# Kernel tuning notes

Measured on AMD Instinct MI355X. Metric: run time of the kernel, lower is better.

## Reference

```python
import jax, jax.numpy as jnp
import numpy as np
import math

VOCAB, D, L, B, S = 32000, 1024, 6, 4, 1024
FF = 4 * D


def sinusoidal_pe(max_len, d_model):
    pos = np.arange(max_len)[:, None].astype(np.float32)
    div = np.exp(np.arange(0, d_model, 2).astype(np.float32) * (-math.log(10000.0) / d_model))
    pe = np.zeros((max_len, d_model), dtype=np.float32)
    pe[:, 0::2] = np.sin(pos * div)
    pe[:, 1::2] = np.cos(pos * div)
    return jnp.asarray(pe)


def layernorm(x, g, b, eps=1e-5):
    mu = jnp.mean(x, axis=-1, keepdims=True)
    var = jnp.mean(jnp.square(x - mu), axis=-1, keepdims=True)
    return (x - mu) * jax.lax.rsqrt(var + eps) * g + b


def setup_inputs() -> dict:
    key = jax.random.key(0)
    ks = jax.random.split(key, 16)
    s = 0.02
    inp = {
        "input_ids": jax.random.randint(ks[0], (B, S), 0, VOCAB, dtype=jnp.int32),
        "attention_mask": jnp.ones((B, S), dtype=jnp.int32),
        "emb": jax.random.normal(ks[1], (VOCAB, D), jnp.float32) * s,
        "Wq": jax.random.normal(ks[2], (L, D, D), jnp.float32) * s,
        "Wk": jax.random.normal(ks[3], (L, D, D), jnp.float32) * s,
        "Wv": jax.random.normal(ks[4], (L, D, D), jnp.float32) * s,
        "bq": jnp.zeros((L, D), jnp.float32),
        "bk": jnp.zeros((L, D), jnp.float32),
        "bv": jnp.zeros((L, D), jnp.float32),
        "g1": jnp.ones((L, D), jnp.float32),
        "beta1": jnp.zeros((L, D), jnp.float32),
        "Wf1": jax.random.normal(ks[5], (L, D, FF), jnp.float32) * s,
        "bf1": jnp.zeros((L, FF), jnp.float32),
        "Wf2": jax.random.normal(ks[6], (L, FF, D), jnp.float32) * s,
        "bf2": jnp.zeros((L, D), jnp.float32),
        "g2": jnp.ones((L, D), jnp.float32),
        "beta2": jnp.zeros((L, D), jnp.float32),
    }
    return inp


def reference(input_ids, attention_mask, emb, Wq, Wk, Wv, bq, bk, bv,
              g1, beta1, Wf1, bf1, Wf2, bf2, g2, beta2):
    pe = sinusoidal_pe(1024, D)
    x = emb[input_ids] + pe[: input_ids.shape[1]]           # [B,S,D]
    mask = (attention_mask[:, None, :] != 0)                # [B,1,S]
    scale = 1.0 / math.sqrt(D)
    for l in range(L):
        Q = jnp.einsum('bsd,de->bse', x, Wq[l]) + bq[l]
        K = jnp.einsum('bsd,de->bse', x, Wk[l]) + bk[l]
        V = jnp.einsum('bsd,de->bse', x, Wv[l]) + bv[l]
        scores = jnp.einsum('bqd,bkd->bqk', Q, K) * scale   # [B,S,S]
        scores = jnp.where(mask, scores, -1e9)
        attn = jax.nn.softmax(scores, axis=-1)
        a = jnp.einsum('bqk,bkd->bqd', attn, V)
        x = layernorm(x + a, g1[l], beta1[l])
        h = jax.nn.relu(jnp.einsum('bsd,df->bsf', x, Wf1[l]) + bf1[l])
        f = jnp.einsum('bsf,fd->bsd', h, Wf2[l]) + bf2[l]
        x = layernorm(x + f, g2[l], beta2[l])
    return x
```

## Files before the change

### kernel.cpp

```cpp
#include <hip/hip_runtime.h>

typedef __bf16 bf16_t;
typedef __bf16 bf16x8 __attribute__((ext_vector_type(8)));
typedef float f32x4 __attribute__((ext_vector_type(4)));
typedef unsigned short u16;

#define DEV static __device__ __forceinline__

DEV float bf2f(u16 u) { __bf16 h = __builtin_bit_cast(__bf16, u); return (float)h; }
DEV u16 f2bf(float f) { __bf16 h = (__bf16)f; return __builtin_bit_cast(u16, h); }

DEV void gll16(bf16_t* lds, const bf16_t* g) {
    __builtin_amdgcn_global_load_lds(
        (const __attribute__((address_space(1))) void*)g,
        (__attribute__((address_space(3))) void*)lds, 16, 0, 0);
}

#define WAITV(N) asm volatile("s_waitcnt vmcnt(" #N ")" ::: "memory")

template <int EPI>
__global__ __launch_bounds__(512, 1)
void gemm8p(const bf16_t* __restrict__ A, int lda,
            const bf16_t* __restrict__ Bt, int ldb,
            bf16_t* __restrict__ C, int ldc,
            const float* __restrict__ bias, int K,
            long kadv, long cadv)
{
    __shared__ bf16_t Asm[2 * 2 * 8192];
    __shared__ bf16_t Bsm[2 * 2 * 8192];
    const int tid = threadIdx.x, w = tid >> 6, l = tid & 63;
    const int z = blockIdx.z;
    A  += (size_t)z * kadv;
    Bt += (size_t)z * kadv;
    C  += (size_t)z * cadv;

    const int gx = gridDim.x;
    int lin = blockIdx.y * gx + blockIdx.x;
    const int nlin = gx * gridDim.y;
    lin = (lin & 7) * (nlin >> 3) + (lin >> 3);
    const size_t row0 = (size_t)(lin / gx) * 256;
    const size_t col0 = (size_t)(lin % gx) * 256;

    const int wr = w >> 2, wc = w & 3;
    const int bh = wc >> 1;
    const int browoff = (wc & 1) * 64;
    const int fr = l & 15, q = l >> 4, sw = l & 7;

    const int srow = w * 8 + (l >> 3);
    const int sslot8 = ((l & 7) ^ ((l >> 3) & 7)) * 8;
    const bf16_t* AgH0 = A  + (row0 + srow) * (size_t)lda + sslot8;
    const bf16_t* BgH0 = Bt + (col0 + srow) * (size_t)ldb + sslot8;
    const size_t a128 = (size_t)128 * lda, b128 = (size_t)128 * ldb;
    const size_t a64  = (size_t)64 * lda,  b64  = (size_t)64 * ldb;
    const int wlds = w * 512;

#define STAGE_PAIR(buf, tt, p)                                                 \
    do {                                                                       \
        const int koff = (tt) * 64;                                            \
        if ((p) == 0) {                                                        \
            gll16(Asm + ((buf)*2+0)*8192 + wlds,        AgH0 + koff);          \
            gll16(Asm + ((buf)*2+0)*8192 + 4096 + wlds, AgH0 + koff + a64);    \
        } else if ((p) == 1) {                                                 \
            gll16(Asm + ((buf)*2+1)*8192 + wlds,        AgH0 + a128 + koff);   \
            gll16(Asm + ((buf)*2+1)*8192 + 4096 + wlds, AgH0 + a128 + koff + a64); \
        } else if ((p) == 2) {                                                 \
            gll16(Bsm + ((buf)*2+0)*8192 + wlds,        BgH0 + koff);          \
            gll16(Bsm + ((buf)*2+0)*8192 + 4096 + wlds, BgH0 + koff + b64);    \
        } else {                                                               \
            gll16(Bsm + ((buf)*2+1)*8192 + wlds,        BgH0 + b128 + koff);   \
            gll16(Bsm + ((buf)*2+1)*8192 + 4096 + wlds, BgH0 + b128 + koff + b64); \
        }                                                                      \
    } while (0)

    f32x4 acc[8][4] = {};
    const int NT = K >> 6;

    STAGE_PAIR(0, 0, 0); STAGE_PAIR(0, 0, 1); STAGE_PAIR(0, 0, 2); STAGE_PAIR(0, 0, 3);
    if (NT > 1) { STAGE_PAIR(1, 1, 0); WAITV(2); } else { WAITV(0); }
    __builtin_amdgcn_sched_barrier(0);
    __builtin_amdgcn_s_barrier();

    for (int t = 0; t < NT; ++t) {
        const int cur = t & 1, nxt = cur ^ 1;
        const bool hasN1 = (t + 1 < NT), hasN2 = (t + 2 < NT);
        const bf16_t* Ab = Asm + (cur * 2 + wr) * 8192;
        const bf16_t* Bb = Bsm + (cur * 2 + bh) * 8192;

        bf16x8 aR[4][2], bR[4][2];
#pragma unroll
        for (int mi = 0; mi < 4; mi++)
#pragma unroll
            for (int kk = 0; kk < 2; kk++)
                aR[mi][kk] = *(const bf16x8*)&Ab[(mi * 16 + fr) * 64 + ((kk * 4 + q) ^ sw) * 8];
#pragma unroll
        for (int ni = 0; ni < 4; ni++)
#pragma unroll
            for (int kk = 0; kk < 2; kk++)
                bR[ni][kk] = *(const bf16x8*)&Bb[(browoff + ni * 16 + fr) * 64 + ((kk * 4 + q) ^ sw) * 8];
        if (hasN1) { STAGE_PAIR(nxt, t + 1, 1); STAGE_PAIR(nxt, t + 1, 2); }
        __builtin_amdgcn_s_setprio(1);
#pragma unroll
        for (int mi = 0; mi < 4; mi++)
#pragma unroll
            for (int ni = 0; ni < 4; ni++)
#pragma unroll
                for (int kk = 0; kk < 2; kk++)
                    acc[mi][ni] = __builtin_amdgcn_mfma_f32_16x16x32_bf16(aR[mi][kk], bR[ni][kk], acc[mi][ni], 0, 0, 0);
        __builtin_amdgcn_s_setprio(0);

        bf16x8 a2[4][2];
#pragma unroll
        for (int mi = 0; mi < 4; mi++)
#pragma unroll
            for (int kk = 0; kk < 2; kk++)
                a2[mi][kk] = *(const bf16x8*)&Ab[((4 + mi) * 16 + fr) * 64 + ((kk * 4 + q) ^ sw) * 8];
        if (hasN1) STAGE_PAIR(nxt, t + 1, 3);
        __builtin_amdgcn_s_setprio(1);
#pragma unroll
        for (int mi = 0; mi < 4; mi++)
#pragma unroll
            for (int ni = 0; ni < 4; ni++)
#pragma unroll
                for (int kk = 0; kk < 2; kk++)
                    acc[4 + mi][ni] = __builtin_amdgcn_mfma_f32_16x16x32_bf16(a2[mi][kk], bR[ni][kk], acc[4 + mi][ni], 0, 0, 0);
        __builtin_amdgcn_s_setprio(0);

        __builtin_amdgcn_s_barrier();
        if (hasN2) STAGE_PAIR(cur, t + 2, 0);
        if (hasN1) {
            if (hasN2) { WAITV(2); } else { WAITV(0); }
            __builtin_amdgcn_sched_barrier(0);
        }
        __builtin_amdgcn_s_barrier();
    }
#undef STAGE_PAIR

    const int cr = q * 4, cc = fr;
#pragma unroll
    for (int ni = 0; ni < 4; ni++) {
        size_t c = col0 + wc * 64 + ni * 16 + cc;
        float bv = bias ? bias[c] : 0.f;
#pragma unroll
        for (int mi = 0; mi < 8; mi++) {
            size_t r = row0 + wr * 128 + mi * 16 + cr;
#pragma unroll
            for (int j = 0; j < 4; j++) {
                float v = acc[mi][ni][j] + bv;
                if (EPI == 1) v = fmaxf(v, 0.f);
                C[(r + j) * ldc + c] = (bf16_t)v;
            }
        }
    }
}

template <int EPI>
__global__ __launch_bounds__(256)
void gemm_db(const bf16_t* __restrict__ A, int lda, long sA,
             const bf16_t* __restrict__ Bt, int ldb, long sB,
             void* __restrict__ Cv, int ldc, long sC,
             const float* __restrict__ bias, int K, float scale)
{
    __shared__ bf16_t Asm[2][128 * 64];
    __shared__ bf16_t Bsm[2][128 * 64];
    const int tid = threadIdx.x, w = tid >> 6, l = tid & 63;
    const int bz = blockIdx.z;

    const int gx = gridDim.x;
    int lin = blockIdx.y * gx + blockIdx.x;
    const int nlin = gx * gridDim.y;
    lin = (lin & 7) * (nlin >> 3) + (lin >> 3);
    const size_t row0 = (size_t)(lin / gx) * 128;
    const size_t col0 = (size_t)(lin % gx) * 128;

    A  += (size_t)bz * sA;
    Bt += (size_t)bz * sB;

    const int lr = l >> 3;
    const int sl = (l & 7) ^ lr;
    const bf16_t* Ag = A  + (row0 + (size_t)(w * 32) + lr) * lda + sl * 8;
    const bf16_t* Bg = Bt + (col0 + (size_t)(w * 32) + lr) * ldb + sl * 8;
    const int wlds = (w * 32) * 64;

#define STA(buf, tt)                                                           \
    do { const int ko = (tt) * 64;                                             \
        _Pragma("unroll")                                                      \
        for (int c = 0; c < 4; c++)                                            \
            gll16(&Asm[buf][wlds + c * 8 * 64], Ag + (size_t)(c * 8) * lda + ko); \
    } while (0)
#define STB(buf, tt)                                                           \
    do { const int ko = (tt) * 64;                                             \
        _Pragma("unroll")                                                      \
        for (int c = 0; c < 4; c++)                                            \
            gll16(&Bsm[buf][wlds + c * 8 * 64], Bg + (size_t)(c * 8) * ldb + ko); \
    } while (0)

    const int wm = (w >> 1) * 64, wn = (w & 1) * 64;
    const int fr16 = l & 15, q4 = l >> 4, sw = l & 7;
    f32x4 acc[4][4] = {};
    const int NT = K >> 6;

    STA(0, 0); STB(0, 0);
    if (NT > 1) { STA(1, 1); WAITV(4); } else { WAITV(0); }
    __builtin_amdgcn_sched_barrier(0);
    __builtin_amdgcn_s_barrier();

    for (int t = 0; t < NT; ++t) {
        const int cur = t & 1, nxt = cur ^ 1;
        const bool hasN1 = (t + 1 < NT), hasN2 = (t + 2 < NT);

        bf16x8 a0[4], b0[4], a1[4], b1[4];
        const int s0 = (q4 ^ sw) * 8, s1 = ((4 + q4) ^ sw) * 8;
#pragma unroll
        for (int i = 0; i < 4; i++) {
            a0[i] = *(const bf16x8*)&Asm[cur][(wm + i * 16 + fr16) * 64 + s0];
            b0[i] = *(const bf16x8*)&Bsm[cur][(wn + i * 16 + fr16) * 64 + s0];
        }
        if (hasN1) STB(nxt, t + 1);
        __builtin_amdgcn_s_setprio(1);
#pragma unroll
        for (int mi = 0; mi < 4; mi++)
#pragma unroll
            for (int ni = 0; ni < 4; ni++)
                acc[mi][ni] = __builtin_amdgcn_mfma_f32_16x16x32_bf16(a0[mi], b0[ni], acc[mi][ni], 0, 0, 0);
        __builtin_amdgcn_s_setprio(0);
#pragma unroll
        for (int i = 0; i < 4; i++) {
            a1[i] = *(const bf16x8*)&Asm[cur][(wm + i * 16 + fr16) * 64 + s1];
            b1[i] = *(const bf16x8*)&Bsm[cur][(wn + i * 16 + fr16) * 64 + s1];
        }
        __builtin_amdgcn_s_setprio(1);
#pragma unroll
        for (int mi = 0; mi < 4; mi++)
#pragma unroll
            for (int ni = 0; ni < 4; ni++)
                acc[mi][ni] = __builtin_amdgcn_mfma_f32_16x16x32_bf16(a1[mi], b1[ni], acc[mi][ni], 0, 0, 0);
        __builtin_amdgcn_s_setprio(0);

        __builtin_amdgcn_s_barrier();
        if (hasN2) STA(cur, t + 2);
        if (hasN1) {
            if (hasN2) { WAITV(4); } else { WAITV(0); }
            __builtin_amdgcn_sched_barrier(0);
        }
        __builtin_amdgcn_s_barrier();
    }
#undef STA
#undef STB

    const int cr = q4 * 4, cc = fr16;
    if (EPI == 2) {
        float* C = (float*)Cv + (size_t)bz * sC;
#pragma unroll
        for (int mi = 0; mi < 4; mi++)
#pragma unroll
            for (int ni = 0; ni < 4; ni++) {
                size_t r = row0 + wm + mi * 16 + cr;
                size_t c = col0 + wn + ni * 16 + cc;
#pragma unroll
                for (int j = 0; j < 4; j++)
                    C[(r + j) * ldc + c] = acc[mi][ni][j] * scale;
            }
    } else {
        bf16_t* C = (bf16_t*)Cv + (size_t)bz * sC;
#pragma unroll
        for (int ni = 0; ni < 4; ni++) {
            size_t c = col0 + wn + ni * 16 + cc;
            float bv = bias ? bias[c] : 0.f;
#pragma unroll
            for (int mi = 0; mi < 4; mi++) {
                size_t r = row0 + wm + mi * 16 + cr;
#pragma unroll
                for (int j = 0; j < 4; j++) {
                    float v = acc[mi][ni][j] + bv;
                    if (EPI == 1) v = fmaxf(v, 0.f);
                    C[(r + j) * ldc + c] = (bf16_t)v;
                }
            }
        }
    }
}

__global__ __launch_bounds__(256)
void prep_kernel(const float* __restrict__ Wq, const float* __restrict__ Wk,
                 const float* __restrict__ Wv, const float* __restrict__ Wf1,
                 const float* __restrict__ Wf2,
                 const float* __restrict__ bq, const float* __restrict__ bk,
                 const float* __restrict__ bv,
                 const int* __restrict__ ids, const float* __restrict__ emb,
                 bf16_t* __restrict__ wqkvTA, bf16_t* __restrict__ wf1TA,
                 bf16_t* __restrict__ wf2TA, float* __restrict__ qbiasA,
                 float* __restrict__ x, bf16_t* __restrict__ xb)
{
    __shared__ bf16_t tls[64][72];
    const size_t DD = 1024 * 1024;
    int id = blockIdx.x;
    if (id < 16896) {
        const float* src; bf16_t* dst; int ldin, ldout, bx, by;
        if (id < 4608) {
            int layer = id / 768, r = id % 768, which = r >> 8, t = r & 255;
            src = (which == 0 ? Wq : which == 1 ? Wk : Wv) + (size_t)layer * DD;
            dst = wqkvTA + (size_t)layer * 3 * DD + (size_t)which * DD;
            ldin = 1024; ldout = 1024; bx = (t & 15) * 64; by = (t >> 4) * 64;
        } else if (id < 10752) {
            int i = id - 4608, layer = i >> 10, t = i & 1023;
            src = Wf1 + (size_t)layer * 4 * DD; dst = wf1TA + (size_t)layer * 4 * DD;
            ldin = 4096; ldout = 1024; bx = (t & 63) * 64; by = (t >> 6) * 64;
        } else {
            int i = id - 10752, layer = i >> 10, t = i & 1023;
            src = Wf2 + (size_t)layer * 4 * DD; dst = wf2TA + (size_t)layer * 4 * DD;
            ldin = 1024; ldout = 4096; bx = (t & 15) * 64; by = (t >> 4) * 64;
        }
        const int tid = threadIdx.x;
        const int cj = (tid & 15) * 4, ri = tid >> 4;
#pragma unroll
        for (int k = 0; k < 4; k++) {
            int r = ri + k * 16;
            float4 v = *(const float4*)&src[(size_t)(by + r) * ldin + bx + cj];
            ushort4 o = {f2bf(v.x), f2bf(v.y), f2bf(v.z), f2bf(v.w)};
            *(ushort4*)&tls[r][cj] = o;
        }
        __syncthreads();
#pragma unroll
        for (int k = 0; k < 4; k++) {
            int i2 = ri + k * 16;
            ushort4 o;
            o.x = __builtin_bit_cast(u16, tls[cj + 0][i2]);
            o.y = __builtin_bit_cast(u16, tls[cj + 1][i2]);
            o.z = __builtin_bit_cast(u16, tls[cj + 2][i2]);
            o.w = __builtin_bit_cast(u16, tls[cj + 3][i2]);
            *(ushort4*)&dst[(size_t)(bx + i2) * ldout + by + cj] = o;
        }
        return;
    }
    id -= 16896;
    if (id < 72) {
        int i = id * 256 + threadIdx.x;
        int lyr = i / 3072, j = i - lyr * 3072;
        qbiasA[i] = (j < 1024) ? bq[lyr * 1024 + j]
                  : (j < 2048) ? bk[lyr * 1024 + j - 1024]
                               : bv[lyr * 1024 + j - 2048];
        return;
    }
    id -= 72;
    const int row = id;
    const int s = row & 1023;
    const int eid = ids[row];
    const float* er = emb + (size_t)eid * 1024;
    float* xr = x + (size_t)row * 1024;
    bf16_t* br = xb + (size_t)row * 1024;
#pragma unroll
    for (int k = 0; k < 2; k++) {
        int i = threadIdx.x + 256 * k;
        int d = 2 * i;
        float dv = expf((float)d * -0.008994473019508f);
        float ph = (float)s * dv;
        float sv, cv;
        sincosf(ph, &sv, &cv);
        float2 ev = *(const float2*)&er[d];
        float x0 = ev.x + sv;
        float x1 = ev.y + cv;
        float2 xo = {x0, x1};
        *(float2*)&xr[d] = xo;
        ushort2 bo = {f2bf(x0), f2bf(x1)};
        *(ushort2*)&br[d] = bo;
    }
}

__global__ __launch_bounds__(256)
void softvt_kernel(const float* __restrict__ sc, const int* __restrict__ amask,
                   bf16_t* __restrict__ p, const bf16_t* __restrict__ qkv,
                   bf16_t* __restrict__ vt)
{
    __shared__ bf16_t tls[64][72];
    int bid = blockIdx.x;
    if (bid < 1024) {
        const int row = bid * 4 + (threadIdx.x >> 6);
        const int l = threadIdx.x & 63;
        const int b = row >> 10;
        const float* s = sc + (size_t)row * 1024;
        const int* m = amask + (size_t)b * 1024;
        float v[16];
        float mx = -3.0e38f;
#pragma unroll
        for (int i = 0; i < 4; i++) {
            int c = 4 * l + 256 * i;
            float4 sv = *(const float4*)&s[c];
            int4 mv = *(const int4*)&m[c];
            v[4 * i + 0] = mv.x ? sv.x : -1e9f;
            v[4 * i + 1] = mv.y ? sv.y : -1e9f;
            v[4 * i + 2] = mv.z ? sv.z : -1e9f;
            v[4 * i + 3] = mv.w ? sv.w : -1e9f;
            mx = fmaxf(mx, fmaxf(fmaxf(v[4 * i], v[4 * i + 1]), fmaxf(v[4 * i + 2], v[4 * i + 3])));
        }
#pragma unroll
        for (int o = 32; o; o >>= 1) mx = fmaxf(mx, __shfl_xor(mx, o, 64));
        float sum = 0.f;
#pragma unroll
        for (int i = 0; i < 16; i++) { v[i] = __expf(v[i] - mx); sum += v[i]; }
#pragma unroll
        for (int o = 32; o; o >>= 1) sum += __shfl_xor(sum, o, 64);
        float inv = 1.0f / sum;
#pragma unroll
        for (int i = 0; i < 4; i++) {
            int c = 4 * l + 256 * i;
            ushort4 st;
            st.x = f2bf(v[4 * i + 0] * inv);
            st.y = f2bf(v[4 * i + 1] * inv);
            st.z = f2bf(v[4 * i + 2] * inv);
            st.w = f2bf(v[4 * i + 3] * inv);
            *(ushort4*)&p[(size_t)row * 1024 + c] = st;
        }
        return;
    }
    bid -= 1024;
    const int z = bid >> 8, t = bid & 255;
    const bf16_t* in = qkv + 2048 + (size_t)z * 1024 * 3072;
    bf16_t* out = vt + (size_t)z * 1024 * 1024;
    const int bx = (t & 15) * 64, by = (t >> 4) * 64;
    const int tid = threadIdx.x;
    const int cj = (tid & 15) * 4, ri = tid >> 4;
#pragma unroll
    for (int k = 0; k < 4; k++) {
        int r = ri + k * 16;
        *(ushort4*)&tls[r][cj] = *(const ushort4*)&in[(size_t)(by + r) * 3072 + bx + cj];
    }
    __syncthreads();
#pragma unroll
    for (int k = 0; k < 4; k++) {
        int i2 = ri + k * 16;
        ushort4 o;
        o.x = __builtin_bit_cast(u16, tls[cj + 0][i2]);
        o.y = __builtin_bit_cast(u16, tls[cj + 1][i2]);
        o.z = __builtin_bit_cast(u16, tls[cj + 2][i2]);
        o.w = __builtin_bit_cast(u16, tls[cj + 3][i2]);
        *(ushort4*)&out[(size_t)(bx + i2) * 1024 + by + cj] = o;
    }
}

__global__ __launch_bounds__(256)
void ln_kernel(const float* __restrict__ xin, const bf16_t* __restrict__ add,
               const float* __restrict__ g, const float* __restrict__ beta,
               float* __restrict__ xout, bf16_t* __restrict__ bout)
{
    __shared__ float red[8];
    const int row = blockIdx.x;
    const int t = threadIdx.x;
    const size_t base = (size_t)row * 1024 + t * 4;
    float4 xv = *(const float4*)&xin[base];
    ushort4 au = *(const ushort4*)&add[base];
    float tv[4];
    tv[0] = xv.x + bf2f(au.x);
    tv[1] = xv.y + bf2f(au.y);
    tv[2] = xv.z + bf2f(au.z);
    tv[3] = xv.w + bf2f(au.w);
    float s = tv[0] + tv[1] + tv[2] + tv[3];
    float s2 = tv[0] * tv[0] + tv[1] * tv[1] + tv[2] * tv[2] + tv[3] * tv[3];
#pragma unroll
    for (int o = 32; o; o >>= 1) { s += __shfl_xor(s, o, 64); s2 += __shfl_xor(s2, o, 64); }
    if ((t & 63) == 0) { red[t >> 6] = s; red[4 + (t >> 6)] = s2; }
    __syncthreads();
    s = red[0] + red[1] + red[2] + red[3];
    s2 = red[4] + red[5] + red[6] + red[7];
    const float mu = s * (1.f / 1024.f);
    const float var = s2 * (1.f / 1024.f) - mu * mu;
    const float rs = rsqrtf(var + 1e-5f);
    float4 gu = *(const float4*)&g[t * 4];
    float4 bu = *(const float4*)&beta[t * 4];
    float y0 = (tv[0] - mu) * rs * gu.x + bu.x;
    float y1 = (tv[1] - mu) * rs * gu.y + bu.y;
    float y2 = (tv[2] - mu) * rs * gu.z + bu.z;
    float y3 = (tv[3] - mu) * rs * gu.w + bu.w;
    float4 yo = {y0, y1, y2, y3};
    *(float4*)&xout[base] = yo;
    ushort4 ob = {f2bf(y0), f2bf(y1), f2bf(y2), f2bf(y3)};
    *(ushort4*)&bout[base] = ob;
}

__global__ __launch_bounds__(256)
void ln4_kernel(const float* __restrict__ xin, const bf16_t* __restrict__ p,
                long pstride, const float* __restrict__ fbias,
                const float* __restrict__ g, const float* __restrict__ beta,
                float* __restrict__ xout, bf16_t* __restrict__ bout)
{
    __shared__ float red[8];
    const int row = blockIdx.x;
    const int t = threadIdx.x;
    const size_t base = (size_t)row * 1024 + t * 4;
    float4 xv = *(const float4*)&xin[base];
    float4 bb = *(const float4*)&fbias[t * 4];
    float tv[4] = {xv.x + bb.x, xv.y + bb.y, xv.z + bb.z, xv.w + bb.w};
#pragma unroll
    for (int z = 0; z < 4; z++) {
        ushort4 au = *(const ushort4*)&p[(size_t)z * pstride + base];
        tv[0] += bf2f(au.x); tv[1] += bf2f(au.y);
        tv[2] += bf2f(au.z); tv[3] += bf2f(au.w);
    }
    float s = tv[0] + tv[1] + tv[2] + tv[3];
    float s2 = tv[0] * tv[0] + tv[1] * tv[1] + tv[2] * tv[2] + tv[3] * tv[3];
#pragma unroll
    for (int o = 32; o; o >>= 1) { s += __shfl_xor(s, o, 64); s2 += __shfl_xor(s2, o, 64); }
    if ((t & 63) == 0) { red[t >> 6] = s; red[4 + (t >> 6)] = s2; }
    __syncthreads();
    s = red[0] + red[1] + red[2] + red[3];
    s2 = red[4] + red[5] + red[6] + red[7];
    const float mu = s * (1.f / 1024.f);
    const float var = s2 * (1.f / 1024.f) - mu * mu;
    const float rs = rsqrtf(var + 1e-5f);
    float4 gu = *(const float4*)&g[t * 4];
    float4 bu = *(const float4*)&beta[t * 4];
    float y0 = (tv[0] - mu) * rs * gu.x + bu.x;
    float y1 = (tv[1] - mu) * rs * gu.y + bu.y;
    float y2 = (tv[2] - mu) * rs * gu.z + bu.z;
    float y3 = (tv[3] - mu) * rs * gu.w + bu.w;
    float4 yo = {y0, y1, y2, y3};
    *(float4*)&xout[base] = yo;
    ushort4 ob = {f2bf(y0), f2bf(y1), f2bf(y2), f2bf(y3)};
    *(ushort4*)&bout[base] = ob;
}


extern "C" void kernel_launch(void* const* d_in, const int* in_sizes, int n_in,
                              void* d_out, int out_size, void* d_ws, size_t ws_size,
                              hipStream_t stream)
{
    const int*   ids = (const int*)d_in[0];
    const int*   am  = (const int*)d_in[1];
    const float* emb = (const float*)d_in[2];
    const float* Wq  = (const float*)d_in[3];
    const float* Wk  = (const float*)d_in[4];
    const float* Wv  = (const float*)d_in[5];
    const float* bq  = (const float*)d_in[6];
    const float* bk  = (const float*)d_in[7];
    const float* bv  = (const float*)d_in[8];
    const float* g1  = (const float*)d_in[9];
    const float* be1 = (const float*)d_in[10];
    const float* Wf1 = (const float*)d_in[11];
    const float* bf1 = (const float*)d_in[12];
    const float* Wf2 = (const float*)d_in[13];
    const float* bf2_ = (const float*)d_in[14];
    const float* g2  = (const float*)d_in[15];
    const float* be2 = (const float*)d_in[16];

    char* ws = (char*)d_ws;
    float*  x      = (float*)(ws);
    bf16_t* xb     = (bf16_t*)(ws + (16LL << 20));
    bf16_t* qkv    = (bf16_t*)(ws + (24LL << 20));
    bf16_t* vt     = (bf16_t*)(ws + (48LL << 20));
    bf16_t* fpart  = (bf16_t*)(ws + (24LL << 20));
    float*  scores = (float*)(ws + (56LL << 20));
    bf16_t* p      = (bf16_t*)(ws + (72LL << 20));
    bf16_t* h      = (bf16_t*)(ws + (56LL << 20));
    bf16_t* attn   = (bf16_t*)(ws + (88LL << 20));
    bf16_t* wqkvTA = (bf16_t*)(ws + (96LL << 20));
    bf16_t* wf1TA  = (bf16_t*)(ws + (132LL << 20));
    bf16_t* wf2TA  = (bf16_t*)(ws + (180LL << 20));
    float*  qbiasA = (float*)(ws + (228LL << 20));

    const size_t DD = 1024 * 1024;

    prep_kernel<<<21064, 256, 0, stream>>>(Wq, Wk, Wv, Wf1, Wf2, bq, bk, bv,
                                           ids, emb, wqkvTA, wf1TA, wf2TA, qbiasA, x, xb);

    for (int l = 0; l < 6; l++) {
        gemm8p<0><<<dim3(12, 16, 1), 512, 0, stream>>>(xb, 1024, wqkvTA + (size_t)l * 3 * DD, 1024,
                                                       qkv, 3072, qbiasA + l * 3072, 1024, 0, 0);
        gemm_db<2><<<dim3(8, 8, 4), 256, 0, stream>>>(qkv, 3072, 1024L * 3072,
                                                      qkv + 1024, 3072, 1024L * 3072,
                                                      scores, 1024, 1024L * 1024,
                                                      nullptr, 1024, 0.03125f);
        softvt_kernel<<<2048, 256, 0, stream>>>(scores, am, p, qkv, vt);
        gemm_db<0><<<dim3(8, 8, 4), 256, 0, stream>>>(p, 1024, 1024L * 1024,
                                                      vt, 1024, 1024L * 1024,
                                                      attn, 1024, 1024L * 1024,
                                                      nullptr, 1024, 0.f);
        ln_kernel<<<4096, 256, 0, stream>>>(x, attn, g1 + l * 1024, be1 + l * 1024, x, xb);
        gemm8p<1><<<dim3(16, 16, 1), 512, 0, stream>>>(xb, 1024, wf1TA + (size_t)l * 4 * DD, 1024,
                                                       h, 4096, bf1 + l * 4096, 1024, 0, 0);
        gemm8p<0><<<dim3(4, 16, 4), 512, 0, stream>>>(h, 4096, wf2TA + (size_t)l * 4 * DD, 4096,
                                                      fpart, 1024, nullptr, 1024,
                                                      1024, 4096L * 1024);
        float* xo = (l == 5) ? (float*)d_out : x;
        ln4_kernel<<<4096, 256, 0, stream>>>(x, fpart, 4096L * 1024, bf2_ + l * 1024,
                                             g2 + l * 1024, be2 + l * 1024, xo, xb);
    }
    (void)in_sizes; (void)n_in; (void)out_size; (void)ws_size;
}
```

Before: 1.274 ms.

## Store attention scores in bf16 and swizzle LDS in weight-prep transpose

The QK^T GEMM now writes scaled scores as bf16 instead of fp32 through a new epilogue, and softmax reads the bf16 scores. This halves the traffic for the scores buffer on write and read. Separately, the prep kernel's transpose tile drops padding and uses an XOR swizzle to avoid LDS bank conflicts. Rounding scores to bf16 before softmax adds precision loss.

```diff
diff --git a/kernel.cpp b/kernel.cpp
--- a/kernel.cpp
+++ b/kernel.cpp
@@ -260,6 +260,18 @@
                 for (int j = 0; j < 4; j++)
                     C[(r + j) * ldc + c] = acc[mi][ni][j] * scale;
             }
+    } else if (EPI == 3) {
+        bf16_t* C = (bf16_t*)Cv + (size_t)bz * sC;
+#pragma unroll
+        for (int mi = 0; mi < 4; mi++)
+#pragma unroll
+            for (int ni = 0; ni < 4; ni++) {
+                size_t r = row0 + wm + mi * 16 + cr;
+                size_t c = col0 + wn + ni * 16 + cc;
+#pragma unroll
+                for (int j = 0; j < 4; j++)
+                    C[(r + j) * ldc + c] = (bf16_t)(acc[mi][ni][j] * scale);
+            }
     } else {
         bf16_t* C = (bf16_t*)Cv + (size_t)bz * sC;
 #pragma unroll
@@ -291,7 +303,7 @@
                  bf16_t* __restrict__ wf2TA, float* __restrict__ qbiasA,
                  float* __restrict__ x, bf16_t* __restrict__ xb)
 {
-    __shared__ bf16_t tls[64][72];
+    __shared__ bf16_t tls[64 * 64];
     const size_t DD = 1024 * 1024;
     int id = blockIdx.x;
     if (id < 16896) {
@@ -311,24 +323,26 @@
             ldin = 1024; ldout = 4096; bx = (t & 15) * 64; by = (t >> 4) * 64;
         }
         const int tid = threadIdx.x;
-        const int cj = (tid & 15) * 4, ri = tid >> 4;
+        const int cg = tid & 15, ri = tid >> 4;
 #pragma unroll
         for (int k = 0; k < 4; k++) {
             int r = ri + k * 16;
-            float4 v = *(const float4*)&src[(size_t)(by + r) * ldin + bx + cj];
+            float4 v = *(const float4*)&src[(size_t)(by + r) * ldin + bx + cg * 4];
             ushort4 o = {f2bf(v.x), f2bf(v.y), f2bf(v.z), f2bf(v.w)};
-            *(ushort4*)&tls[r][cj] = o;
+            int g = cg ^ ((r >> 2) & 15);
+            *(ushort4*)&tls[r * 64 + g * 4] = o;
         }
         __syncthreads();
 #pragma unroll
         for (int k = 0; k < 4; k++) {
             int i2 = ri + k * 16;
+            int gr = (i2 >> 2) ^ cg;
             ushort4 o;
-            o.x = __builtin_bit_cast(u16, tls[cj + 0][i2]);
-            o.y = __builtin_bit_cast(u16, tls[cj + 1][i2]);
-            o.z = __builtin_bit_cast(u16, tls[cj + 2][i2]);
-            o.w = __builtin_bit_cast(u16, tls[cj + 3][i2]);
-            *(ushort4*)&dst[(size_t)(bx + i2) * ldout + by + cj] = o;
+            o.x = __builtin_bit_cast(u16, tls[(cg * 4 + 0) * 64 + gr * 4 + (i2 & 3)]);
+            o.y = __builtin_bit_cast(u16, tls[(cg * 4 + 1) * 64 + gr * 4 + (i2 & 3)]);
+            o.z = __builtin_bit_cast(u16, tls[(cg * 4 + 2) * 64 + gr * 4 + (i2 & 3)]);
+            o.w = __builtin_bit_cast(u16, tls[(cg * 4 + 3) * 64 + gr * 4 + (i2 & 3)]);
+            *(ushort4*)&dst[(size_t)(bx + i2) * ldout + by + cg * 4] = o;
         }
         return;
     }
@@ -367,7 +381,7 @@
 }
 
 __global__ __launch_bounds__(256)
-void softvt_kernel(const float* __restrict__ sc, const int* __restrict__ amask,
+void softvt_kernel(const bf16_t* __restrict__ sc, const int* __restrict__ amask,
                    bf16_t* __restrict__ p, const bf16_t* __restrict__ qkv,
                    bf16_t* __restrict__ vt)
 {
@@ -377,19 +391,19 @@
         const int row = bid * 4 + (threadIdx.x >> 6);
         const int l = threadIdx.x & 63;
         const int b = row >> 10;
-        const float* s = sc + (size_t)row * 1024;
+        const bf16_t* s = sc + (size_t)row * 1024;
         const int* m = amask + (size_t)b * 1024;
         float v[16];
         float mx = -3.0e38f;
 #pragma unroll
         for (int i = 0; i < 4; i++) {
             int c = 4 * l + 256 * i;
-            float4 sv = *(const float4*)&s[c];
+            ushort4 su = *(const ushort4*)&s[c];
             int4 mv = *(const int4*)&m[c];
-            v[4 * i + 0] = mv.x ? sv.x : -1e9f;
-            v[4 * i + 1] = mv.y ? sv.y : -1e9f;
-            v[4 * i + 2] = mv.z ? sv.z : -1e9f;
-            v[4 * i + 3] = mv.w ? sv.w : -1e9f;
+            v[4 * i + 0] = mv.x ? bf2f(su.x) : -1e9f;
+            v[4 * i + 1] = mv.y ? bf2f(su.y) : -1e9f;
+            v[4 * i + 2] = mv.z ? bf2f(su.z) : -1e9f;
+            v[4 * i + 3] = mv.w ? bf2f(su.w) : -1e9f;
             mx = fmaxf(mx, fmaxf(fmaxf(v[4 * i], v[4 * i + 1]), fmaxf(v[4 * i + 2], v[4 * i + 3])));
         }
 #pragma unroll
@@ -547,7 +561,7 @@
     bf16_t* qkv    = (bf16_t*)(ws + (24LL << 20));
     bf16_t* vt     = (bf16_t*)(ws + (48LL << 20));
     bf16_t* fpart  = (bf16_t*)(ws + (24LL << 20));
-    float*  scores = (float*)(ws + (56LL << 20));
+    bf16_t* scores = (bf16_t*)(ws + (56LL << 20));
     bf16_t* p      = (bf16_t*)(ws + (72LL << 20));
     bf16_t* h      = (bf16_t*)(ws + (56LL << 20));
     bf16_t* attn   = (bf16_t*)(ws + (88LL << 20));
@@ -564,7 +578,7 @@
     for (int l = 0; l < 6; l++) {
         gemm8p<0><<<dim3(12, 16, 1), 512, 0, stream>>>(xb, 1024, wqkvTA + (size_t)l * 3 * DD, 1024,
                                                        qkv, 3072, qbiasA + l * 3072, 1024, 0, 0);
-        gemm_db<2><<<dim3(8, 8, 4), 256, 0, stream>>>(qkv, 3072, 1024L * 3072,
+        gemm_db<3><<<dim3(8, 8, 4), 256, 0, stream>>>(qkv, 3072, 1024L * 3072,
                                                       qkv + 1024, 3072, 1024L * 3072,
                                                       scores, 1024, 1024L * 1024,
                                                       nullptr, 1024, 0.03125f);
```

Result: no change. 1.262 ms (-0.9%).
